# Kernel optimization log

Hardware: AMD Instinct MI355X
Metric: run time of the kernel (lower is better)

The kernel has to match this reference:

```python
import jax, jax.numpy as jnp
from jax import lax
import numpy as np

ALPHA = 0.5      # convex-combination rate from __init__ default
DECAY = 0.9
B, IN, H, OUT, K = 8192, 512, 512, 256, 3


def setup_inputs() -> dict:
    key = jax.random.key(0)
    ks = jax.random.split(key, 8)
    sc = 1.0 / np.sqrt(IN)
    sh = 1.0 / np.sqrt(H)
    return {
        "x": jax.random.normal(ks[0], (B, IN), jnp.float32),
        "Wx_w": jax.random.normal(ks[1], (H, IN), jnp.float32) * sc,
        "Wx_b": jax.random.normal(ks[2], (H,), jnp.float32) * sc,
        # orthogonal-ish, scaled by 0.9 like nn.init.orthogonal_ + mul_(0.9)
        "Wh_w": 0.9 * jnp.linalg.qr(jax.random.normal(ks[3], (H, H), jnp.float32))[0],
        "Wh_b": jax.random.normal(ks[4], (H,), jnp.float32) * sh,
        "Head_w": jax.random.normal(ks[5], (OUT, H), jnp.float32) * sh,
        "Head_b": jax.random.normal(ks[6], (OUT,), jnp.float32) * sh,
        "buffer_gamma": jnp.asarray(0.1, jnp.float32),
        "alphas": jnp.asarray([DECAY ** (k + 1) for k in range(K)], jnp.float32),
        "steps": 30,
    }


def reference(x, Wx_w, Wx_b, Wh_w, Wh_b, Head_w, Head_b, buffer_gamma, alphas, steps):
    batch = x.shape[0]
    hidden = Wh_w.shape[0]
    k_hist = alphas.shape[0]
    # Wx(x) is constant across steps -> hoist out of the loop (same math)
    xproj = x @ Wx_w.T + Wx_b                      # [B, H]
    stack0 = jnp.zeros((batch, k_hist + 1, hidden), x.dtype)  # [B, K+1, H]

    def step(stack, _):
        s_t = stack[:, 0]                          # [B, H]
        history = stack[:, 1:]                     # [B, K, H]
        recirc = jnp.einsum('bkh,k->bh', history, alphas)
        pre_act = xproj + s_t @ Wh_w.T + Wh_b + buffer_gamma * recirc
        h_new = jnp.tanh(pre_act)
        s_next = (1.0 - ALPHA) * s_t + ALPHA * h_new
        new_stack = jnp.concatenate(
            [s_next[:, None], s_t[:, None], history[:, :-1]], axis=1)
        return new_stack, None

    stack, _ = lax.scan(step, stack0, None, length=steps)
    return stack[:, 0] @ Head_w.T + Head_b         # [B, OUT]
```

## Files before the change

### kernel.cpp

```cpp
#include <hip/hip_runtime.h>
#include <hip/hip_bf16.h>

typedef __attribute__((ext_vector_type(8))) short short8;
typedef __attribute__((ext_vector_type(4))) float f32x4;

#define THREADS 512
#define MFMA(a, b, c) __builtin_amdgcn_mfma_f32_16x16x32_bf16((a), (b), (c), 0, 0, 0)

static __device__ __forceinline__ unsigned short f2bf(float x) {
    __hip_bfloat16 h = __float2bfloat16(x);
    return __builtin_bit_cast(unsigned short, h);
}
static __device__ __forceinline__ unsigned pk2(float a, float b) {
    return (unsigned)f2bf(a) | ((unsigned)f2bf(b) << 16);
}
static __device__ __forceinline__ float bflo(unsigned u) {
    unsigned v = u << 16; return __builtin_bit_cast(float, v);
}
static __device__ __forceinline__ float bfhi(unsigned u) {
    unsigned v = u & 0xffff0000u; return __builtin_bit_cast(float, v);
}
static __device__ __forceinline__ float fast_tanh(float x) {
    float e = __builtin_amdgcn_exp2f(x * 2.885390081777927f);
    float r = __builtin_amdgcn_rcpf(e + 1.0f);
    return fmaf(-2.0f, r, 1.0f);
}
static __device__ __forceinline__ short8 cvt8(float4 a, float4 b) {
    short8 r;
    r[0] = (short)f2bf(a.x); r[1] = (short)f2bf(a.y);
    r[2] = (short)f2bf(a.z); r[3] = (short)f2bf(a.w);
    r[4] = (short)f2bf(b.x); r[5] = (short)f2bf(b.y);
    r[6] = (short)f2bf(b.z); r[7] = (short)f2bf(b.w);
    return r;
}
static __device__ __forceinline__ void gl_lds16(const unsigned short* g, unsigned short* l) {
    __builtin_amdgcn_global_load_lds(
        (const __attribute__((address_space(1))) unsigned int*)g,
        (__attribute__((address_space(3))) unsigned int*)l, 16, 0, 1);
}
static __device__ __forceinline__ int ldf(int* p) {
    return __hip_atomic_load(p, __ATOMIC_RELAXED, __HIP_MEMORY_SCOPE_AGENT);
}
static __device__ __forceinline__ void stf(int* p, int v) {
    __hip_atomic_store(p, v, __ATOMIC_RELAXED, __HIP_MEMORY_SCOPE_AGENT);
}
#define WAITV0() asm volatile("s_waitcnt vmcnt(0)" ::: "memory")

#define LOAD_PANEL(W, CB, KT_OF_J)                                              \
    do {                                                                        \
        _Pragma("unroll")                                                       \
        for (int j = 0; j < 16; ++j) {                                          \
            const int kt_ = (KT_OF_J);                                          \
            const float* p0_ = (W) + (size_t)((CB) + c) * 512 + kt_ * 32 + q * 8;       \
            const float* p1_ = (W) + (size_t)((CB) + 16 + c) * 512 + kt_ * 32 + q * 8;  \
            float4 a0_ = *(const float4*)p0_, b0_ = *(const float4*)(p0_ + 4);  \
            float4 a1_ = *(const float4*)p1_, b1_ = *(const float4*)(p1_ + 4);  \
            bw0[j] = cvt8(a0_, b0_);                                            \
            bw1[j] = cvt8(a1_, b1_);                                            \
        }                                                                       \
    } while (0)

__global__ __attribute__((amdgpu_flat_work_group_size(512, 512), amdgpu_waves_per_eu(2, 2)))
void toroidal(
    const float* __restrict__ x,
    const float* __restrict__ Wx_w, const float* __restrict__ wxb,
    const float* __restrict__ Wh_w, const float* __restrict__ whb,
    const float* __restrict__ Hd_w, const float* __restrict__ hdb,
    const float* __restrict__ gamma_p, const float* __restrict__ alphas,
    const int* __restrict__ steps_p,
    float* __restrict__ out, int* __restrict__ flags)
{
    __shared__ __align__(16) unsigned short sfrag[32768];
    __shared__ __align__(16) unsigned int   hist[16384];

    const int tid = threadIdx.x;
    const int w = tid >> 6;
    const int l = tid & 63;
    const int q = l >> 4;
    const int c = l & 15;

    const int bi  = blockIdx.x;
    const int mu  = (bi >> 3) & 1;
    const int grp = (bi & 7) * 16 + (bi >> 4);
    const int pb  = bi ^ 8;
    const int rows0 = grp * 64;

    int* prod = flags;
    int* cons = flags + 256;

    unsigned short* piece_me = (unsigned short*)out + (size_t)grp * 32768 + mu * 16384;
    unsigned short* piece_pa = (unsigned short*)out + (size_t)grp * 32768 + (1 - mu) * 16384;

    const float gm = gamma_p[0];
    const float g1 = gm * alphas[0], g2 = gm * alphas[1], g3 = gm * alphas[2];
    const int nsteps = steps_p[0];

    const int colbase = mu * 256 + w * 32;
    const float bias0 = wxb[colbase + c] + whb[colbase + c];
    const float bias1 = wxb[colbase + 16 + c] + whb[colbase + 16 + c];
    const float hb0 = hdb[w * 32 + c], hb1 = hdb[w * 32 + 16 + c];

    const int roff = l * 8;
    const int k0own = 8 * mu, k0par = 8 * (1 - mu);

    short8 bw0[16], bw1[16];

    LOAD_PANEL(Wx_w, colbase, j);

    f32x4 acc[4][2];
    #pragma unroll
    for (int mt = 0; mt < 4; ++mt) {
        acc[mt][0] = (f32x4){0.f, 0.f, 0.f, 0.f};
        acc[mt][1] = (f32x4){0.f, 0.f, 0.f, 0.f};
    }
    #pragma unroll
    for (int pass = 0; pass < 2; ++pass) {
        __syncthreads();
        #pragma unroll
        for (int j2 = 0; j2 < 8; ++j2) {
            int r = j2 * 8 + w;
            int kloc = l * 4;
            float4 v = *(const float4*)(x + (size_t)(rows0 + r) * 512 + pass * 256 + kloc);
            int mtx = r >> 4, ktl = kloc >> 5;
            int lane2 = (r & 15) + 16 * ((kloc >> 3) & 3);
            float* dst = (float*)sfrag + ((mtx * 8 + ktl) * 64 + lane2) * 8 + (kloc & 7);
            *(float4*)dst = v;
        }
        __syncthreads();
        #pragma unroll
        for (int j = 0; j < 8; ++j) {
            #pragma unroll
            for (int mt = 0; mt < 4; ++mt) {
                const float* fp = (const float*)sfrag + ((mt * 8 + j) * 64 + l) * 8;
                float4 u0 = *(const float4*)fp;
                float4 u1 = *(const float4*)(fp + 4);
                short8 a = cvt8(u0, u1);
                acc[mt][0] = MFMA(a, bw0[pass * 8 + j], acc[mt][0]);
                acc[mt][1] = MFMA(a, bw1[pass * 8 + j], acc[mt][1]);
            }
        }
    }
    __syncthreads();

    unsigned xpk[4][2][2];
    #pragma unroll
    for (int mt = 0; mt < 4; ++mt)
        #pragma unroll
        for (int nt = 0; nt < 2; ++nt) {
            float b = nt ? bias1 : bias0;
            xpk[mt][nt][0] = pk2(acc[mt][nt][0] + b, acc[mt][nt][1] + b);
            xpk[mt][nt][1] = pk2(acc[mt][nt][2] + b, acc[mt][nt][3] + b);
        }

    LOAD_PANEL(Wh_w, colbase, (j < 8 ? k0own + j : k0par + (j - 8)));

    uint4 z4 = {0u, 0u, 0u, 0u};
    #pragma unroll
    for (int sb = 0; sb < 8; ++sb) *(uint4*)&hist[(sb * 512 + tid) * 4] = z4;
    float s[4][2][4];
    unsigned h0[4][2][2];
    #pragma unroll
    for (int mt = 0; mt < 4; ++mt)
        #pragma unroll
        for (int nt = 0; nt < 2; ++nt) {
            acc[mt][nt] = (f32x4){0.f, 0.f, 0.f, 0.f};
            h0[mt][nt][0] = h0[mt][nt][1] = 0u;
            #pragma unroll
            for (int i = 0; i < 4; ++i) s[mt][nt][i] = 0.f;
        }

    for (int t = 1; t <= nsteps; ++t) {
        const int sA = t & 1, sB = sA ^ 1;
        #pragma unroll
        for (int mt = 0; mt < 4; ++mt) {
            uint4 hA = *(uint4*)&hist[((sA * 4 + mt) * 512 + tid) * 4];
            uint4 hB = *(uint4*)&hist[((sB * 4 + mt) * 512 + tid) * 4];
            uint4 nB;
            #pragma unroll
            for (int nt = 0; nt < 2; ++nt)
                #pragma unroll
                for (int pi = 0; pi < 2; ++pi) {
                    unsigned u1 = h0[mt][nt][pi];
                    unsigned u2 = ((unsigned*)&hA)[nt * 2 + pi];
                    unsigned u3 = ((unsigned*)&hB)[nt * 2 + pi];
                    unsigned ux = xpk[mt][nt][pi];
                    float p0 = acc[mt][nt][pi * 2] + bflo(ux)
                             + g1 * bflo(u1) + g2 * bflo(u2) + g3 * bflo(u3);
                    float p1 = acc[mt][nt][pi * 2 + 1] + bfhi(ux)
                             + g1 * bfhi(u1) + g2 * bfhi(u2) + g3 * bfhi(u3);
                    float so0 = s[mt][nt][pi * 2], so1 = s[mt][nt][pi * 2 + 1];
                    float sn0 = 0.5f * so0 + 0.5f * fast_tanh(p0);
                    float sn1 = 0.5f * so1 + 0.5f * fast_tanh(p1);
                    s[mt][nt][pi * 2] = sn0; s[mt][nt][pi * 2 + 1] = sn1;
                    ((unsigned*)&nB)[nt * 2 + pi] = u1;
                    h0[mt][nt][pi] = pk2(so0, so1);
                }
            *(uint4*)&hist[((sB * 4 + mt) * 512 + tid) * 4] = nB;
            acc[mt][0] = (f32x4){0.f, 0.f, 0.f, 0.f};
            acc[mt][1] = (f32x4){0.f, 0.f, 0.f, 0.f};
        }

        if (l == 0) { while (ldf(&cons[pb]) < t - 1) __builtin_amdgcn_s_sleep(1); }
        __builtin_amdgcn_sched_barrier(0);

        #pragma unroll
        for (int mt = 0; mt < 4; ++mt)
            #pragma unroll
            for (int nt = 0; nt < 2; ++nt)
                #pragma unroll
                for (int i = 0; i < 4; ++i) {
                    int lam = q * 4 + i + 16 * (nt * 2 + (c >> 3));
                    sfrag[(mt * 16 + k0own + w) * 512 + lam * 8 + (c & 7)] = f2bf(s[mt][nt][i]);
                }
        __syncthreads();

        #pragma unroll
        for (int j2 = 0; j2 < 4; ++j2) {
            int u = j2 * 512 + tid;
            int mtg = u >> 9, ktl = (u >> 6) & 7, co = (u & 63) * 8;
            uint4 v = *(const uint4*)&sfrag[(mtg * 16 + k0own + ktl) * 512 + co];
            *(uint4*)&piece_me[(size_t)u * 8] = v;
        }

        if (t == nsteps) {
            WAITV0();
            __builtin_amdgcn_s_barrier();
            if (tid == 0) stf(&prod[bi], t);
            break;
        }

        #pragma unroll
        for (int j = 0; j < 8; ++j) {
            const int kt = k0own + j;
            short8 a0 = *(const short8*)&sfrag[(0 * 16 + kt) * 512 + roff];
            short8 a1 = *(const short8*)&sfrag[(1 * 16 + kt) * 512 + roff];
            short8 a2 = *(const short8*)&sfrag[(2 * 16 + kt) * 512 + roff];
            short8 a3 = *(const short8*)&sfrag[(3 * 16 + kt) * 512 + roff];
            acc[0][0] = MFMA(a0, bw0[j], acc[0][0]); acc[0][1] = MFMA(a0, bw1[j], acc[0][1]);
            acc[1][0] = MFMA(a1, bw0[j], acc[1][0]); acc[1][1] = MFMA(a1, bw1[j], acc[1][1]);
            acc[2][0] = MFMA(a2, bw0[j], acc[2][0]); acc[2][1] = MFMA(a2, bw1[j], acc[2][1]);
            acc[3][0] = MFMA(a3, bw0[j], acc[3][0]); acc[3][1] = MFMA(a3, bw1[j], acc[3][1]);
        }

        WAITV0();
        __builtin_amdgcn_s_barrier();
        if (tid == 0) stf(&prod[bi], t);

        if (l == 0) { while (ldf(&prod[pb]) < t) __builtin_amdgcn_s_sleep(1); }
        __builtin_amdgcn_sched_barrier(0);
        {
            const int mtg = w >> 1;
            #pragma unroll
            for (int i2 = 0; i2 < 4; ++i2) {
                const int ktl = 4 * (w & 1) + i2;
                gl_lds16(piece_pa + (mtg * 8 + ktl) * 512 + l * 8,
                         &sfrag[(mtg * 16 + k0par + ktl) * 512]);
            }
        }
        __syncthreads();
        if (tid == 0) stf(&cons[bi], t);

        #pragma unroll
        for (int j = 8; j < 16; ++j) {
            const int kt = k0par + (j - 8);
            short8 a0 = *(const short8*)&sfrag[(0 * 16 + kt) * 512 + roff];
            short8 a1 = *(const short8*)&sfrag[(1 * 16 + kt) * 512 + roff];
            short8 a2 = *(const short8*)&sfrag[(2 * 16 + kt) * 512 + roff];
            short8 a3 = *(const short8*)&sfrag[(3 * 16 + kt) * 512 + roff];
            acc[0][0] = MFMA(a0, bw0[j], acc[0][0]); acc[0][1] = MFMA(a0, bw1[j], acc[0][1]);
            acc[1][0] = MFMA(a1, bw0[j], acc[1][0]); acc[1][1] = MFMA(a1, bw1[j], acc[1][1]);
            acc[2][0] = MFMA(a2, bw0[j], acc[2][0]); acc[2][1] = MFMA(a2, bw1[j], acc[2][1]);
            acc[3][0] = MFMA(a3, bw0[j], acc[3][0]); acc[3][1] = MFMA(a3, bw1[j], acc[3][1]);
        }
    }

    if (l == 0) { while (ldf(&prod[pb]) < nsteps) __builtin_amdgcn_s_sleep(1); }
    __builtin_amdgcn_sched_barrier(0);
    {
        const int mtg = w >> 1;
        #pragma unroll
        for (int i2 = 0; i2 < 4; ++i2) {
            const int ktl = 4 * (w & 1) + i2;
            gl_lds16(piece_pa + (mtg * 8 + ktl) * 512 + l * 8,
                     &sfrag[(mtg * 16 + k0par + ktl) * 512]);
        }
    }
    LOAD_PANEL(Hd_w, w * 32, (j < 8 ? k0own + j : k0par + (j - 8)));
    __syncthreads();
    if (tid == 0) stf(&cons[bi], nsteps);

    f32x4 ah[2][2];
    ah[0][0] = (f32x4){0.f, 0.f, 0.f, 0.f}; ah[0][1] = (f32x4){0.f, 0.f, 0.f, 0.f};
    ah[1][0] = (f32x4){0.f, 0.f, 0.f, 0.f}; ah[1][1] = (f32x4){0.f, 0.f, 0.f, 0.f};
    #pragma unroll
    for (int j = 0; j < 16; ++j) {
        const int kt = (j < 8) ? k0own + j : k0par + (j - 8);
        short8 a0 = *(const short8*)&sfrag[((2 * mu + 0) * 16 + kt) * 512 + roff];
        short8 a1 = *(const short8*)&sfrag[((2 * mu + 1) * 16 + kt) * 512 + roff];
        ah[0][0] = MFMA(a0, bw0[j], ah[0][0]); ah[0][1] = MFMA(a0, bw1[j], ah[0][1]);
        ah[1][0] = MFMA(a1, bw0[j], ah[1][0]); ah[1][1] = MFMA(a1, bw1[j], ah[1][1]);
    }

    if (l == 0) { while (ldf(&cons[pb]) < nsteps) __builtin_amdgcn_s_sleep(1); }
    __builtin_amdgcn_sched_barrier(0);
    #pragma unroll
    for (int mtL = 0; mtL < 2; ++mtL)
        #pragma unroll
        for (int i = 0; i < 4; ++i) {
            int r = rows0 + 32 * mu + mtL * 16 + q * 4 + i;
            out[(size_t)r * 256 + w * 32 + c]      = ah[mtL][0][i] + hb0;
            out[(size_t)r * 256 + w * 32 + 16 + c] = ah[mtL][1][i] + hb1;
        }
}

extern "C" void kernel_launch(void* const* d_in, const int* in_sizes, int n_in,
                              void* d_out, int out_size, void* d_ws, size_t ws_size,
                              hipStream_t stream) {
    (void)n_in; (void)out_size;
    const float* x    = (const float*)d_in[0];
    const float* Wx_w = (const float*)d_in[1];
    const float* Wx_b = (const float*)d_in[2];
    const float* Wh_w = (const float*)d_in[3];
    const float* Wh_b = (const float*)d_in[4];
    const float* Hd_w = (const float*)d_in[5];
    const float* Hd_b = (const float*)d_in[6];
    const float* gma  = (const float*)d_in[7];
    const float* alp  = (const float*)d_in[8];
    const int*   stp  = (const int*)d_in[9];
    float* out = (float*)d_out;

    if (ws_size < 4096) return;
    int* flags = (int*)d_ws;
    hipMemsetAsync(flags, 0, 4096, stream);

    int batch = in_sizes[0] / 512;
    int nblk  = batch / 32;
    toroidal<<<nblk, THREADS, 0, stream>>>(x, Wx_w, Wx_b, Wh_w, Wh_b, Hd_w, Hd_b,
                                           gma, alp, stp, out, flags);
}
```

Baseline: 643.2 us.

## Double-buffer partner exchange pieces in workspace to drop consumer-ack handshake

Moves the per-step state exchange between paired blocks from the output buffer into a workspace area and, when the workspace is large enough, alternates between two slots by step parity. This removes the wait on the partner's consumer flag before each publish, leaving one flag wait per step. The exchange now uses 64-bit system-scope atomic stores and loads staged through registers instead of global-to-LDS loads, and the sleep interval in the spin loops is doubled. System-scope atomics may bypass caches and cost more per access. The double-buffered path depends on the workspace size available at runtime.

```diff
diff --git a/kernel.cpp b/kernel.cpp
--- a/kernel.cpp
+++ b/kernel.cpp
@@ -3,6 +3,7 @@
 
 typedef __attribute__((ext_vector_type(8))) short short8;
 typedef __attribute__((ext_vector_type(4))) float f32x4;
+typedef unsigned long long u64;
 
 #define THREADS 512
 #define MFMA(a, b, c) __builtin_amdgcn_mfma_f32_16x16x32_bf16((a), (b), (c), 0, 0, 0)
@@ -33,16 +34,17 @@
     r[6] = (short)f2bf(b.z); r[7] = (short)f2bf(b.w);
     return r;
 }
-static __device__ __forceinline__ void gl_lds16(const unsigned short* g, unsigned short* l) {
-    __builtin_amdgcn_global_load_lds(
-        (const __attribute__((address_space(1))) unsigned int*)g,
-        (__attribute__((address_space(3))) unsigned int*)l, 16, 0, 1);
-}
-static __device__ __forceinline__ int ldf(int* p) {
-    return __hip_atomic_load(p, __ATOMIC_RELAXED, __HIP_MEMORY_SCOPE_AGENT);
+static __device__ __forceinline__ u64 ld_sys(const u64* p) {
+    return __hip_atomic_load(p, __ATOMIC_RELAXED, __HIP_MEMORY_SCOPE_SYSTEM);
+}
+static __device__ __forceinline__ void st_sys(u64* p, u64 v) {
+    __hip_atomic_store(p, v, __ATOMIC_RELAXED, __HIP_MEMORY_SCOPE_SYSTEM);
+}
+static __device__ __forceinline__ int ldf(const int* p) {
+    return __hip_atomic_load(p, __ATOMIC_RELAXED, __HIP_MEMORY_SCOPE_SYSTEM);
 }
 static __device__ __forceinline__ void stf(int* p, int v) {
-    __hip_atomic_store(p, v, __ATOMIC_RELAXED, __HIP_MEMORY_SCOPE_AGENT);
+    __hip_atomic_store(p, v, __ATOMIC_RELAXED, __HIP_MEMORY_SCOPE_SYSTEM);
 }
 #define WAITV0() asm volatile("s_waitcnt vmcnt(0)" ::: "memory")
 
@@ -60,6 +62,7 @@
         }                                                                       \
     } while (0)
 
+template<bool DBUF>
 __global__ __attribute__((amdgpu_flat_work_group_size(512, 512), amdgpu_waves_per_eu(2, 2)))
 void toroidal(
     const float* __restrict__ x,
@@ -68,7 +71,8 @@
     const float* __restrict__ Hd_w, const float* __restrict__ hdb,
     const float* __restrict__ gamma_p, const float* __restrict__ alphas,
     const int* __restrict__ steps_p,
-    float* __restrict__ out, int* __restrict__ flags)
+    float* __restrict__ out, int* __restrict__ flags,
+    unsigned short* __restrict__ pieces, size_t slotStride )
 {
     __shared__ __align__(16) unsigned short sfrag[32768];
     __shared__ __align__(16) unsigned int   hist[16384];
@@ -88,8 +92,8 @@
     int* prod = flags;
     int* cons = flags + 256;
 
-    unsigned short* piece_me = (unsigned short*)out + (size_t)grp * 32768 + mu * 16384;
-    unsigned short* piece_pa = (unsigned short*)out + (size_t)grp * 32768 + (1 - mu) * 16384;
+    unsigned short* pbase = pieces + (size_t)grp * 32768 + mu * 16384;
+    const unsigned short* qbase = pieces + (size_t)grp * 32768 + (1 - mu) * 16384;
 
     const float gm = gamma_p[0];
     const float g1 = gm * alphas[0], g2 = gm * alphas[1], g3 = gm * alphas[2];
@@ -200,9 +204,6 @@
             acc[mt][1] = (f32x4){0.f, 0.f, 0.f, 0.f};
         }
 
-        if (l == 0) { while (ldf(&cons[pb]) < t - 1) __builtin_amdgcn_s_sleep(1); }
-        __builtin_amdgcn_sched_barrier(0);
-
         #pragma unroll
         for (int mt = 0; mt < 4; ++mt)
             #pragma unroll
@@ -214,12 +215,18 @@
                 }
         __syncthreads();
 
-        #pragma unroll
-        for (int j2 = 0; j2 < 4; ++j2) {
-            int u = j2 * 512 + tid;
-            int mtg = u >> 9, ktl = (u >> 6) & 7, co = (u & 63) * 8;
-            uint4 v = *(const uint4*)&sfrag[(mtg * 16 + k0own + ktl) * 512 + co];
-            *(uint4*)&piece_me[(size_t)u * 8] = v;
+        if (!DBUF) {
+            if (l == 0) { while (ldf(&cons[pb]) < t - 1) __builtin_amdgcn_s_sleep(2); }
+            __builtin_amdgcn_sched_barrier(0);
+        }
+
+        u64* dstp = (u64*)(pbase + (DBUF ? (size_t)(t & 1) * slotStride : 0));
+        #pragma unroll
+        for (int i = 0; i < 8; ++i) {
+            int u = i * 512 + tid;
+            int mtg = u >> 10, ktl = (u >> 7) & 7, off = (u & 127) * 4;
+            u64 v = *(const u64*)&sfrag[(mtg * 16 + k0own + ktl) * 512 + off];
+            st_sys(dstp + u, v);
         }
 
         if (t == nsteps) {
@@ -246,19 +253,22 @@
         __builtin_amdgcn_s_barrier();
         if (tid == 0) stf(&prod[bi], t);
 
-        if (l == 0) { while (ldf(&prod[pb]) < t) __builtin_amdgcn_s_sleep(1); }
+        if (l == 0) { while (ldf(&prod[pb]) < t) __builtin_amdgcn_s_sleep(2); }
         __builtin_amdgcn_sched_barrier(0);
         {
-            const int mtg = w >> 1;
-            #pragma unroll
-            for (int i2 = 0; i2 < 4; ++i2) {
-                const int ktl = 4 * (w & 1) + i2;
-                gl_lds16(piece_pa + (mtg * 8 + ktl) * 512 + l * 8,
-                         &sfrag[(mtg * 16 + k0par + ktl) * 512]);
+            const u64* srcp = (const u64*)(qbase + (DBUF ? (size_t)(t & 1) * slotStride : 0));
+            u64 tmp[8];
+            #pragma unroll
+            for (int i = 0; i < 8; ++i) tmp[i] = ld_sys(srcp + i * 512 + tid);
+            #pragma unroll
+            for (int i = 0; i < 8; ++i) {
+                int u = i * 512 + tid;
+                int mtg = u >> 10, ktl = (u >> 7) & 7, off = (u & 127) * 4;
+                *(u64*)&sfrag[(mtg * 16 + k0par + ktl) * 512 + off] = tmp[i];
             }
         }
         __syncthreads();
-        if (tid == 0) stf(&cons[bi], t);
+        if (!DBUF) { if (tid == 0) stf(&cons[bi], t); }
 
         #pragma unroll
         for (int j = 8; j < 16; ++j) {
@@ -274,20 +284,23 @@
         }
     }
 
-    if (l == 0) { while (ldf(&prod[pb]) < nsteps) __builtin_amdgcn_s_sleep(1); }
+    if (l == 0) { while (ldf(&prod[pb]) < nsteps) __builtin_amdgcn_s_sleep(2); }
     __builtin_amdgcn_sched_barrier(0);
     {
-        const int mtg = w >> 1;
-        #pragma unroll
-        for (int i2 = 0; i2 < 4; ++i2) {
-            const int ktl = 4 * (w & 1) + i2;
-            gl_lds16(piece_pa + (mtg * 8 + ktl) * 512 + l * 8,
-                     &sfrag[(mtg * 16 + k0par + ktl) * 512]);
+        const u64* srcp = (const u64*)(qbase + (DBUF ? (size_t)(nsteps & 1) * slotStride : 0));
+        u64 tmp[8];
+        #pragma unroll
+        for (int i = 0; i < 8; ++i) tmp[i] = ld_sys(srcp + i * 512 + tid);
+        #pragma unroll
+        for (int i = 0; i < 8; ++i) {
+            int u = i * 512 + tid;
+            int mtg = u >> 10, ktl = (u >> 7) & 7, off = (u & 127) * 4;
+            *(u64*)&sfrag[(mtg * 16 + k0par + ktl) * 512 + off] = tmp[i];
         }
     }
     LOAD_PANEL(Hd_w, w * 32, (j < 8 ? k0own + j : k0par + (j - 8)));
     __syncthreads();
-    if (tid == 0) stf(&cons[bi], nsteps);
+    if (!DBUF) { if (tid == 0) stf(&cons[bi], nsteps); }
 
     f32x4 ah[2][2];
     ah[0][0] = (f32x4){0.f, 0.f, 0.f, 0.f}; ah[0][1] = (f32x4){0.f, 0.f, 0.f, 0.f};
@@ -301,8 +314,10 @@
         ah[1][0] = MFMA(a1, bw0[j], ah[1][0]); ah[1][1] = MFMA(a1, bw1[j], ah[1][1]);
     }
 
-    if (l == 0) { while (ldf(&cons[pb]) < nsteps) __builtin_amdgcn_s_sleep(1); }
-    __builtin_amdgcn_sched_barrier(0);
+    if (!DBUF) {
+        if (l == 0) { while (ldf(&cons[pb]) < nsteps) __builtin_amdgcn_s_sleep(2); }
+        __builtin_amdgcn_sched_barrier(0);
+    }
     #pragma unroll
     for (int mtL = 0; mtL < 2; ++mtL)
         #pragma unroll
@@ -333,8 +348,23 @@
     int* flags = (int*)d_ws;
     hipMemsetAsync(flags, 0, 4096, stream);
 
+    const size_t SLOT = (size_t)8 << 20;
     int batch = in_sizes[0] / 512;
     int nblk  = batch / 32;
-    toroidal<<<nblk, THREADS, 0, stream>>>(x, Wx_w, Wx_b, Wh_w, Wh_b, Hd_w, Hd_b,
-                                           gma, alp, stp, out, flags);
-}
+
+    if (ws_size >= 4096 + 2 * SLOT) {
+        unsigned short* pieces = (unsigned short*)((char*)d_ws + 4096);
+        toroidal<true><<<nblk, THREADS, 0, stream>>>(x, Wx_w, Wx_b, Wh_w, Wh_b, Hd_w, Hd_b,
+                                                     gma, alp, stp, out, flags,
+                                                     pieces, SLOT / 2);
+    } else if (ws_size >= 4096 + SLOT) {
+        unsigned short* pieces = (unsigned short*)((char*)d_ws + 4096);
+        toroidal<false><<<nblk, THREADS, 0, stream>>>(x, Wx_w, Wx_b, Wh_w, Wh_b, Hd_w, Hd_b,
+                                                      gma, alp, stp, out, flags,
+                                                      pieces, 0);
+    } else {
+        toroidal<false><<<nblk, THREADS, 0, stream>>>(x, Wx_w, Wx_b, Wh_w, Wh_b, Hd_w, Hd_b,
+                                                      gma, alp, stp, out, flags,
+                                                      (unsigned short*)out, 0);
+    }
+}
```

New measurement: 574.1 us. 10.7% less time.
